# Performance work log

Measured on AMD Instinct MI355X. Metric: run time of the kernel, lower is better.

The kernel has to match this reference:

```python
import jax, jax.numpy as jnp
import numpy as np

E = 1_000_000
NODE_IN = 64
EDGE_IN = 32
GLOBAL_IN = 32
HIDDEN = 128
EDGE_OUT = 32
B = 128


def setup_inputs() -> dict:
    key = jax.random.key(0)
    ks = jax.random.split(key, 10)
    src = jax.random.normal(ks[0], (E, NODE_IN), dtype=jnp.float32)
    dest = jax.random.normal(ks[1], (E, NODE_IN), dtype=jnp.float32)
    edge_attr = jax.random.normal(ks[2], (E, EDGE_IN), dtype=jnp.float32)
    u = jax.random.normal(ks[3], (B, GLOBAL_IN), dtype=jnp.float32)
    edge_batch = jnp.sort(jax.random.randint(ks[4], (E,), 0, B, dtype=jnp.int32)).astype(jnp.int64)
    in_dim = EDGE_IN + 2 * NODE_IN + GLOBAL_IN  # 192
    # Kaiming-uniform-ish init scale, values irrelevant for correctness baseline
    W1 = jax.random.normal(ks[5], (in_dim, HIDDEN), dtype=jnp.float32) * (1.0 / np.sqrt(in_dim))
    b1 = jnp.zeros((HIDDEN,), dtype=jnp.float32)
    W2 = jax.random.normal(ks[6], (HIDDEN, EDGE_OUT), dtype=jnp.float32) * (1.0 / np.sqrt(HIDDEN))
    b2 = jnp.zeros((EDGE_OUT,), dtype=jnp.float32)
    return {"src": src, "dest": dest, "edge_attr": edge_attr, "u": u,
            "edge_batch": edge_batch, "W1": W1, "b1": b1, "W2": W2, "b2": b2}


def reference(src, dest, edge_attr, u, edge_batch, W1, b1, W2, b2):
    # gather per-edge global features: [E, global_in_dim]
    u_expanded = u[edge_batch]
    # concat -> [E, edge_in + 2*node_in + global_in]
    combined = jnp.concatenate([src, dest, edge_attr, u_expanded], axis=1)
    # 2-layer MLP with ReLU
    h = jax.nn.relu(combined @ W1 + b1)
    out = h @ W2 + b2
    return out
```

## Files before the change

### kernel.cpp

```cpp
#include <hip/hip_runtime.h>

#define NODE_IN 64
#define EDGE_IN 32
#define GLOBAL_IN 32
#define HID 128
#define EOUT 32

typedef float f32x4 __attribute__((ext_vector_type(4)));
typedef short s16x8 __attribute__((ext_vector_type(8)));
typedef unsigned short u16x4 __attribute__((ext_vector_type(4)));

__device__ __forceinline__ unsigned short f2bf(float f) {
  unsigned int u = __float_as_uint(f);
  u += 0x7FFFu + ((u >> 16) & 1u);
  return (unsigned short)(u >> 16);
}

__device__ __forceinline__ u16x4 cvt4(f32x4 v) {
  u16x4 r = { f2bf(v[0]), f2bf(v[1]), f2bf(v[2]), f2bf(v[3]) };
  return r;
}

__global__ __launch_bounds__(256) void edge_mlp(
    const float* __restrict__ srcp, const float* __restrict__ dstp,
    const float* __restrict__ eap, const float* __restrict__ up,
    const int* __restrict__ ebp, const float* __restrict__ W1,
    const float* __restrict__ b1, const float* __restrict__ W2,
    const float* __restrict__ b2, float* __restrict__ outp,
    int E, int ntiles)
{
  __shared__ __align__(16) unsigned short Xl[64][200];
  __shared__ __align__(16) unsigned short Hl[64][136];

  const int t = threadIdx.x;
  const int wid = t >> 6;
  const int lane = t & 63;
  const int g = lane >> 4;
  const int r16 = lane & 15;

  s16x8 w1f[6][2];
#pragma unroll
  for (int kk = 0; kk < 6; ++kk) {
#pragma unroll
    for (int nt = 0; nt < 2; ++nt) {
      s16x8 v;
#pragma unroll
      for (int j = 0; j < 8; ++j) {
        v[j] = (short)f2bf(W1[(32*kk + 8*g + j)*HID + 32*wid + 16*nt + r16]);
      }
      w1f[kk][nt] = v;
    }
  }
  s16x8 w2f[4][2];
#pragma unroll
  for (int kk = 0; kk < 4; ++kk) {
#pragma unroll
    for (int nt = 0; nt < 2; ++nt) {
      s16x8 v;
#pragma unroll
      for (int j = 0; j < 8; ++j) {
        v[j] = (short)f2bf(W2[(32*kk + 8*g + j)*EOUT + 16*nt + r16]);
      }
      w2f[kk][nt] = v;
    }
  }
  const float b1v0 = b1[32*wid + r16];
  const float b1v1 = b1[32*wid + 16 + r16];
  const float b2v0 = b2[r16];
  const float b2v1 = b2[16 + r16];

  for (int tile = blockIdx.x; tile < ntiles; tile += gridDim.x) {
    const int mbase = tile * 64;

#pragma unroll
    for (int i = 0; i < 4; ++i) {
      const int idx = t + 256*i;
      const int row = idx >> 4, c4 = idx & 15;
      int grow = mbase + row; grow = grow < E ? grow : (E - 1);
      const f32x4 vs = *(const f32x4*)(srcp + (size_t)grow*NODE_IN + c4*4);
      *(u16x4*)&Xl[row][c4*4] = cvt4(vs);
      const f32x4 vd = *(const f32x4*)(dstp + (size_t)grow*NODE_IN + c4*4);
      *(u16x4*)&Xl[row][NODE_IN + c4*4] = cvt4(vd);
    }
#pragma unroll
    for (int i = 0; i < 2; ++i) {
      const int idx = t + 256*i;
      const int row = idx >> 3, c4 = idx & 7;
      int grow = mbase + row; grow = grow < E ? grow : (E - 1);
      const f32x4 ve = *(const f32x4*)(eap + (size_t)grow*EDGE_IN + c4*4);
      *(u16x4*)&Xl[row][2*NODE_IN + c4*4] = cvt4(ve);
      const int bb = ebp[grow];
      const f32x4 vu = *(const f32x4*)(up + (size_t)bb*GLOBAL_IN + c4*4);
      *(u16x4*)&Xl[row][2*NODE_IN + EDGE_IN + c4*4] = cvt4(vu);
    }
    __syncthreads();

    f32x4 acc[4][2];
    {
      const f32x4 z = {0.f, 0.f, 0.f, 0.f};
#pragma unroll
      for (int mi = 0; mi < 4; ++mi) { acc[mi][0] = z; acc[mi][1] = z; }
    }
#pragma unroll
    for (int kk = 0; kk < 6; ++kk) {
#pragma unroll
      for (int mi = 0; mi < 4; ++mi) {
        const s16x8 a = *(const s16x8*)&Xl[16*mi + r16][32*kk + 8*g];
        acc[mi][0] = __builtin_amdgcn_mfma_f32_16x16x32_bf16(a, w1f[kk][0], acc[mi][0], 0, 0, 0);
        acc[mi][1] = __builtin_amdgcn_mfma_f32_16x16x32_bf16(a, w1f[kk][1], acc[mi][1], 0, 0, 0);
      }
    }
#pragma unroll
    for (int mi = 0; mi < 4; ++mi) {
#pragma unroll
      for (int j = 0; j < 4; ++j) {
        const float h0 = fmaxf(acc[mi][0][j] + b1v0, 0.f);
        const float h1 = fmaxf(acc[mi][1][j] + b1v1, 0.f);
        Hl[16*mi + 4*g + j][32*wid + r16]      = f2bf(h0);
        Hl[16*mi + 4*g + j][32*wid + 16 + r16] = f2bf(h1);
      }
    }
    __syncthreads();

    f32x4 acc2[2];
    {
      const f32x4 z = {0.f, 0.f, 0.f, 0.f};
      acc2[0] = z; acc2[1] = z;
    }
#pragma unroll
    for (int kk = 0; kk < 4; ++kk) {
      const s16x8 a = *(const s16x8*)&Hl[16*wid + r16][32*kk + 8*g];
      acc2[0] = __builtin_amdgcn_mfma_f32_16x16x32_bf16(a, w2f[kk][0], acc2[0], 0, 0, 0);
      acc2[1] = __builtin_amdgcn_mfma_f32_16x16x32_bf16(a, w2f[kk][1], acc2[1], 0, 0, 0);
    }
#pragma unroll
    for (int j = 0; j < 4; ++j) {
      const int m = mbase + 16*wid + 4*g + j;
      if (m < E) {
        outp[(size_t)m*EOUT + r16]      = acc2[0][j] + b2v0;
        outp[(size_t)m*EOUT + 16 + r16] = acc2[1][j] + b2v1;
      }
    }
  }
}

extern "C" void kernel_launch(void* const* d_in, const int* in_sizes, int n_in,
                              void* d_out, int out_size, void* d_ws, size_t ws_size,
                              hipStream_t stream) {
  const float* srcp = (const float*)d_in[0];
  const float* dstp = (const float*)d_in[1];
  const float* eap  = (const float*)d_in[2];
  const float* up   = (const float*)d_in[3];
  const int*   ebp  = (const int*)d_in[4];
  const float* W1   = (const float*)d_in[5];
  const float* b1   = (const float*)d_in[6];
  const float* W2   = (const float*)d_in[7];
  const float* b2   = (const float*)d_in[8];
  float* outp = (float*)d_out;

  const int E = in_sizes[0] / NODE_IN;
  const int ntiles = (E + 63) / 64;
  const int grid = ntiles < 2048 ? ntiles : 2048;

  edge_mlp<<<grid, 256, 0, stream>>>(srcp, dstp, eap, up, ebp, W1, b1, W2, b2,
                                     outp, E, ntiles);
}
```

Baseline: 165.0 us.

## Share one LDS buffer, interleave output columns, widen staging loads and stores

Merges the X and H shared-memory tiles into one aliased buffer and adds barriers to protect the reuse, cutting LDS per block so more blocks can be resident, and requests 4 blocks per CU in the launch bounds. Permutes the weight columns so each lane owns two adjacent output columns. This lets H be written as packed 32-bit words and the output as 8-byte stores. Input staging switches to 8-element chunks with 16-byte LDS writes, and bf16 conversion uses the native cast. The cost is two extra barriers per tile and a tighter register budget.

```diff
diff --git a/kernel.cpp b/kernel.cpp
--- a/kernel.cpp
+++ b/kernel.cpp
@@ -7,21 +7,25 @@
 #define EOUT 32
 
 typedef float f32x4 __attribute__((ext_vector_type(4)));
+typedef float f32x2 __attribute__((ext_vector_type(2)));
 typedef short s16x8 __attribute__((ext_vector_type(8)));
-typedef unsigned short u16x4 __attribute__((ext_vector_type(4)));
+typedef unsigned short u16x8 __attribute__((ext_vector_type(8)));
 
 __device__ __forceinline__ unsigned short f2bf(float f) {
-  unsigned int u = __float_as_uint(f);
-  u += 0x7FFFu + ((u >> 16) & 1u);
-  return (unsigned short)(u >> 16);
+  __bf16 h = (__bf16)f;
+  return __builtin_bit_cast(unsigned short, h);
 }
 
-__device__ __forceinline__ u16x4 cvt4(f32x4 v) {
-  u16x4 r = { f2bf(v[0]), f2bf(v[1]), f2bf(v[2]), f2bf(v[3]) };
-  return r;
+__device__ __forceinline__ void stage8(const float* __restrict__ p,
+                                       unsigned short* dst) {
+  const f32x4 a = *(const f32x4*)p;
+  const f32x4 b = *(const f32x4*)(p + 4);
+  u16x8 v = { f2bf(a[0]), f2bf(a[1]), f2bf(a[2]), f2bf(a[3]),
+              f2bf(b[0]), f2bf(b[1]), f2bf(b[2]), f2bf(b[3]) };
+  *(u16x8*)dst = v;
 }
 
-__global__ __launch_bounds__(256) void edge_mlp(
+__global__ __launch_bounds__(256, 4) void edge_mlp(
     const float* __restrict__ srcp, const float* __restrict__ dstp,
     const float* __restrict__ eap, const float* __restrict__ up,
     const int* __restrict__ ebp, const float* __restrict__ W1,
@@ -29,8 +33,7 @@
     const float* __restrict__ b2, float* __restrict__ outp,
     int E, int ntiles)
 {
-  __shared__ __align__(16) unsigned short Xl[64][200];
-  __shared__ __align__(16) unsigned short Hl[64][136];
+  __shared__ __align__(16) unsigned short SM[64 * 200];
 
   const int t = threadIdx.x;
   const int wid = t >> 6;
@@ -45,9 +48,8 @@
     for (int nt = 0; nt < 2; ++nt) {
       s16x8 v;
 #pragma unroll
-      for (int j = 0; j < 8; ++j) {
-        v[j] = (short)f2bf(W1[(32*kk + 8*g + j)*HID + 32*wid + 16*nt + r16]);
-      }
+      for (int j = 0; j < 8; ++j)
+        v[j] = (short)f2bf(W1[(32*kk + 8*g + j)*HID + 32*wid + 2*r16 + nt]);
       w1f[kk][nt] = v;
     }
   }
@@ -58,40 +60,39 @@
     for (int nt = 0; nt < 2; ++nt) {
       s16x8 v;
 #pragma unroll
-      for (int j = 0; j < 8; ++j) {
-        v[j] = (short)f2bf(W2[(32*kk + 8*g + j)*EOUT + 16*nt + r16]);
-      }
+      for (int j = 0; j < 8; ++j)
+        v[j] = (short)f2bf(W2[(32*kk + 8*g + j)*EOUT + 2*r16 + nt]);
       w2f[kk][nt] = v;
     }
   }
-  const float b1v0 = b1[32*wid + r16];
-  const float b1v1 = b1[32*wid + 16 + r16];
-  const float b2v0 = b2[r16];
-  const float b2v1 = b2[16 + r16];
+  const float b1v0 = b1[32*wid + 2*r16];
+  const float b1v1 = b1[32*wid + 2*r16 + 1];
+  const float b2v0 = b2[2*r16];
+  const float b2v1 = b2[2*r16 + 1];
 
   for (int tile = blockIdx.x; tile < ntiles; tile += gridDim.x) {
     const int mbase = tile * 64;
 
 #pragma unroll
-    for (int i = 0; i < 4; ++i) {
-      const int idx = t + 256*i;
-      const int row = idx >> 4, c4 = idx & 15;
-      int grow = mbase + row; grow = grow < E ? grow : (E - 1);
-      const f32x4 vs = *(const f32x4*)(srcp + (size_t)grow*NODE_IN + c4*4);
-      *(u16x4*)&Xl[row][c4*4] = cvt4(vs);
-      const f32x4 vd = *(const f32x4*)(dstp + (size_t)grow*NODE_IN + c4*4);
-      *(u16x4*)&Xl[row][NODE_IN + c4*4] = cvt4(vd);
+    for (int k = 0; k < 2; ++k) {
+      const int cid = t + 256*k;
+      const int row = cid >> 3, c = cid & 7;
+      const int grow = min(mbase + row, E - 1);
+      stage8(srcp + (size_t)grow*NODE_IN + 8*c, &SM[row*200 + 8*c]);
     }
 #pragma unroll
-    for (int i = 0; i < 2; ++i) {
-      const int idx = t + 256*i;
-      const int row = idx >> 3, c4 = idx & 7;
-      int grow = mbase + row; grow = grow < E ? grow : (E - 1);
-      const f32x4 ve = *(const f32x4*)(eap + (size_t)grow*EDGE_IN + c4*4);
-      *(u16x4*)&Xl[row][2*NODE_IN + c4*4] = cvt4(ve);
+    for (int k = 0; k < 2; ++k) {
+      const int cid = t + 256*k;
+      const int row = cid >> 3, c = cid & 7;
+      const int grow = min(mbase + row, E - 1);
+      stage8(dstp + (size_t)grow*NODE_IN + 8*c, &SM[row*200 + 64 + 8*c]);
+    }
+    {
+      const int row = t >> 2, c = t & 3;
+      const int grow = min(mbase + row, E - 1);
+      stage8(eap + (size_t)grow*EDGE_IN + 8*c, &SM[row*200 + 128 + 8*c]);
       const int bb = ebp[grow];
-      const f32x4 vu = *(const f32x4*)(up + (size_t)bb*GLOBAL_IN + c4*4);
-      *(u16x4*)&Xl[row][2*NODE_IN + EDGE_IN + c4*4] = cvt4(vu);
+      stage8(up + (size_t)bb*GLOBAL_IN + 8*c, &SM[row*200 + 160 + 8*c]);
     }
     __syncthreads();
 
@@ -105,19 +106,22 @@
     for (int kk = 0; kk < 6; ++kk) {
 #pragma unroll
       for (int mi = 0; mi < 4; ++mi) {
-        const s16x8 a = *(const s16x8*)&Xl[16*mi + r16][32*kk + 8*g];
+        const s16x8 a = *(const s16x8*)&SM[(16*mi + r16)*200 + 32*kk + 8*g];
         acc[mi][0] = __builtin_amdgcn_mfma_f32_16x16x32_bf16(a, w1f[kk][0], acc[mi][0], 0, 0, 0);
         acc[mi][1] = __builtin_amdgcn_mfma_f32_16x16x32_bf16(a, w1f[kk][1], acc[mi][1], 0, 0, 0);
       }
     }
+    __syncthreads();
+
 #pragma unroll
     for (int mi = 0; mi < 4; ++mi) {
 #pragma unroll
       for (int j = 0; j < 4; ++j) {
         const float h0 = fmaxf(acc[mi][0][j] + b1v0, 0.f);
         const float h1 = fmaxf(acc[mi][1][j] + b1v1, 0.f);
-        Hl[16*mi + 4*g + j][32*wid + r16]      = f2bf(h0);
-        Hl[16*mi + 4*g + j][32*wid + 16 + r16] = f2bf(h1);
+        const unsigned int pk = (unsigned int)f2bf(h0) |
+                                ((unsigned int)f2bf(h1) << 16);
+        *(unsigned int*)&SM[(16*mi + 4*g + j)*136 + 32*wid + 2*r16] = pk;
       }
     }
     __syncthreads();
@@ -129,7 +133,7 @@
     }
 #pragma unroll
     for (int kk = 0; kk < 4; ++kk) {
-      const s16x8 a = *(const s16x8*)&Hl[16*wid + r16][32*kk + 8*g];
+      const s16x8 a = *(const s16x8*)&SM[(16*wid + r16)*136 + 32*kk + 8*g];
       acc2[0] = __builtin_amdgcn_mfma_f32_16x16x32_bf16(a, w2f[kk][0], acc2[0], 0, 0, 0);
       acc2[1] = __builtin_amdgcn_mfma_f32_16x16x32_bf16(a, w2f[kk][1], acc2[1], 0, 0, 0);
     }
@@ -137,10 +141,11 @@
     for (int j = 0; j < 4; ++j) {
       const int m = mbase + 16*wid + 4*g + j;
       if (m < E) {
-        outp[(size_t)m*EOUT + r16]      = acc2[0][j] + b2v0;
-        outp[(size_t)m*EOUT + 16 + r16] = acc2[1][j] + b2v1;
+        f32x2 o = { acc2[0][j] + b2v0, acc2[1][j] + b2v1 };
+        *(f32x2*)(outp + (size_t)m*EOUT + 2*r16) = o;
       }
     }
+    __syncthreads();
   }
 }
 
```

Result: slower. 209.7 us (+27.1%).
